# Kernel optimization log

Hardware: AMD Instinct MI355X
Metric: run time of the kernel (lower is better)

The kernel has to match this reference:

```python
import jax, jax.numpy as jnp
import numpy as np

B, S, D, M = 4, 8192, 1024, 512  # batch, seq_len, dim, memory_dim (= dim // 2)
LN_EPS = 1e-5


def _layernorm(z, g, b):
    mu = jnp.mean(z, axis=-1, keepdims=True)
    var = jnp.var(z, axis=-1, keepdims=True)
    return (z - mu) * jax.lax.rsqrt(var + LN_EPS) * g + b


def setup_inputs() -> dict:
    key = jax.random.key(0)
    ks = jax.random.split(key, 16)
    s_d = 1.0 / np.sqrt(D)
    s_m = 1.0 / np.sqrt(M)
    return {
        "x": jax.random.normal(ks[0], (B, S, D), jnp.float32),
        "Wd": jax.random.normal(ks[1], (D, M), jnp.float32) * s_d,
        "bd": jnp.zeros((M,), jnp.float32),
        "Wq": jax.random.normal(ks[2], (M, M), jnp.float32) * s_m,
        "bq": jnp.zeros((M,), jnp.float32),
        "Wk": jax.random.normal(ks[3], (M, M), jnp.float32) * s_m,
        "bk": jnp.zeros((M,), jnp.float32),
        "Wv": jax.random.normal(ks[4], (M, M), jnp.float32) * s_m,
        "bv": jnp.zeros((M,), jnp.float32),
        "gq": jnp.ones((M,), jnp.float32),
        "bq_ln": jnp.zeros((M,), jnp.float32),
        "gk": jnp.ones((M,), jnp.float32),
        "bk_ln": jnp.zeros((M,), jnp.float32),
        "W1": jax.random.normal(ks[5], (M, M), jnp.float32) * s_m,  # MemoryMLP layer 1
        "W2": jax.random.normal(ks[6], (M, M), jnp.float32) * s_m,  # MemoryMLP layer 2
        "Wu": jax.random.normal(ks[7], (M, D), jnp.float32) * s_m,
        "bu": jnp.zeros((D,), jnp.float32),
        "adaptive_lr": jnp.float32(0.01),
        "forget_factor": jnp.float32(0.1),
    }


def reference(x, Wd, bd, Wq, bq, Wk, bk, Wv, bv, gq, bq_ln, gk, bk_ln,
              W1, W2, Wu, bu, adaptive_lr, forget_factor):
    # project to memory dim: [B,S,M]
    h = jnp.einsum('bsd,dm->bsm', x, Wd) + bd
    q = _layernorm(h @ Wq + bq, gq, bq_ln)
    k = _layernorm(h @ Wk + bk, gk, bk_ln)
    v = h @ Wv + bv
    # MemoryMLP prediction on keys (depth 2, gelu between)
    pred = jax.nn.gelu(k @ W1) @ W2
    # surprise (negative gradient direction of MSE store loss), lr-scaled
    u = adaptive_lr * (v - pred)                       # inputs to scan [B,S,M]
    g = jax.nn.sigmoid(forget_factor)                  # scalar retention gate
    gates = jnp.full((B, S, 1), g, dtype=x.dtype)
    # gated linear recurrence s_t = g_t * s_{t-1} + u_t  (AssocScan math)
    def combine(a, c):
        g1, u1 = a
        g2, u2 = c
        return (g1 * g2, u1 * g2 + u2)
    _, mem = jax.lax.associative_scan(combine, (gates, u), axis=1)  # [B,S,M]
    # query-gated readout, project up, residual ('mal' integration)
    retrieved = q * mem
    out = x + jnp.einsum('bsm,md->bsd', retrieved, Wu) + bu
    return out
```

## Files before the change

kernel.cpp:

```cpp
#include <hip/hip_runtime.h>
#include <hip/hip_bf16.h>
#include <cstdint>


typedef unsigned short u16;
typedef unsigned int u32;
typedef __attribute__((ext_vector_type(8))) short short8;
typedef __attribute__((ext_vector_type(4))) float f32x4;

#define R_ROWS 32768
#define S_LEN 8192
#define D_DIM 1024
#define M_DIM 512

__device__ __forceinline__ float bf2f(u16 u) {
  union { unsigned int i; float f; } v; v.i = ((unsigned int)u) << 16; return v.f;
}
__device__ __forceinline__ u16 f2bf(float f) {
  union { float f; unsigned int i; } v; v.f = f;
  unsigned int r = v.i + 0x7fff + ((v.i >> 16) & 1);
  return (u16)(r >> 16);
}

__global__ __launch_bounds__(256)
void conv_f2b(const float* __restrict__ src, u16* __restrict__ dst) {
  const long i = ((long)blockIdx.x * 256 + threadIdx.x) * 8;
  short8 o;
#pragma unroll
  for (int j = 0; j < 8; ++j) o[j] = (short)f2bf(src[i + j]);
  *(short8*)(dst + i) = o;
}

__global__ __launch_bounds__(256)
void transpose_f2b(const float* __restrict__ src, u16* __restrict__ dst,
                   int rows, int cols) {
  __shared__ u16 tile[32][33];
  const int tx = threadIdx.x & 31;
  const int ty = threadIdx.x >> 5;
  const int bx = blockIdx.x, by = blockIdx.y;
  const int c = bx * 32 + tx;
#pragma unroll
  for (int i = 0; i < 32; i += 8)
    tile[ty + i][tx] = f2bf(src[(long)(by * 32 + ty + i) * cols + c]);
  __syncthreads();
  const int c2 = by * 32 + tx;
#pragma unroll
  for (int i = 0; i < 32; i += 8)
    dst[(long)(bx * 32 + ty + i) * rows + c2] = tile[tx][ty + i];
}

__global__ __launch_bounds__(256)
void concat3(const float* __restrict__ a, const float* __restrict__ b,
             const float* __restrict__ c, float* __restrict__ o) {
  const int i = blockIdx.x * 256 + threadIdx.x;
  o[i] = (i < 512) ? a[i] : (i < 1024) ? b[i - 512] : c[i - 1024];
}

template <int EPI>
__global__ __launch_bounds__(256, 2)
void gemm_bt(const u16* __restrict__ A, const u16* __restrict__ BT,
             const float* __restrict__ bias, void* __restrict__ Cv,
             const int K, const int N,
             const void* __restrict__ auxv, const float* __restrict__ sclr) {
  __shared__ __align__(16) short As[128 * 32];
  __shared__ __align__(16) short Bs[128 * 32];
  const int tid = threadIdx.x;
  const int lane = tid & 63;
  const int wid = tid >> 6;
  const int l15 = lane & 15;
  const int lg = lane >> 4;
  const int wr = wid >> 1;
  const int wc = wid & 1;
  const long am0 = (long)blockIdx.x * 128;
  const long bn0 = (long)blockIdx.y * 128;
  const int srow = tid >> 2;
  const int scol = (tid & 3) * 8;

  f32x4 acc[4][4];
#pragma unroll
  for (int i = 0; i < 4; ++i)
#pragma unroll
    for (int j = 0; j < 4; ++j) acc[i][j] = (f32x4){0.f, 0.f, 0.f, 0.f};

  for (int k0 = 0; k0 < K; k0 += 32) {
#pragma unroll
    for (int p = 0; p < 2; ++p) {
      const u16* ga = A + (am0 + p * 64 + srow) * K + (k0 + scol);
      const u16* gb = BT + (bn0 + p * 64 + srow) * K + (k0 + scol);
      char* la = ((char*)As) + p * 4096 + wid * 1024;
      char* lb = ((char*)Bs) + p * 4096 + wid * 1024;
      __builtin_amdgcn_global_load_lds(
          (const __attribute__((address_space(1))) void*)ga,
          (__attribute__((address_space(3))) void*)la, 16, 0, 0);
      __builtin_amdgcn_global_load_lds(
          (const __attribute__((address_space(1))) void*)gb,
          (__attribute__((address_space(3))) void*)lb, 16, 0, 0);
    }
    __syncthreads();
    short8 af[4], bf[4];
#pragma unroll
    for (int mi = 0; mi < 4; ++mi)
      af[mi] = *(const short8*)(As + (wr * 64 + mi * 16 + l15) * 32 + lg * 8);
#pragma unroll
    for (int ni = 0; ni < 4; ++ni)
      bf[ni] = *(const short8*)(Bs + (wc * 64 + ni * 16 + l15) * 32 + lg * 8);
#pragma unroll
    for (int mi = 0; mi < 4; ++mi)
#pragma unroll
      for (int ni = 0; ni < 4; ++ni)
        acc[mi][ni] = __builtin_amdgcn_mfma_f32_16x16x32_bf16(
            af[mi], bf[ni], acc[mi][ni], 0, 0, 0);
    __syncthreads();
  }

  if constexpr (EPI == 3) {
    __shared__ float Cs[32 * 132];
    const u16* xb = (const u16*)auxv;
    float* Of = (float*)Cv;
    const int trow = tid >> 5;
    const int tcol = (tid & 31) * 4;
#pragma unroll
    for (int p = 0; p < 4; ++p) {
      __syncthreads();
      if (wr == (p >> 1)) {
        const int mbase = (p & 1) * 2;
#pragma unroll
        for (int mm = 0; mm < 2; ++mm)
#pragma unroll
          for (int ni = 0; ni < 4; ++ni)
#pragma unroll
            for (int r = 0; r < 4; ++r)
              Cs[(mm * 16 + lg * 4 + r) * 132 + wc * 64 + ni * 16 + l15] =
                  acc[mbase + mm][ni][r];
      }
      __syncthreads();
#pragma unroll
      for (int rb = 0; rb < 32; rb += 8) {
        const int lrow = rb + trow;
        const long row = am0 + p * 32 + lrow;
        const long col = bn0 + tcol;
        f32x4 cv = *(const f32x4*)&Cs[lrow * 132 + tcol];
        const u32* xp = (const u32*)(xb + row * N + col);
        const u32 x0 = xp[0], x1 = xp[1];
        const f32x4 bv = *(const f32x4*)&bias[col];
        cv[0] += bf2f((u16)(x0 & 0xffff)) + bv[0];
        cv[1] += bf2f((u16)(x0 >> 16)) + bv[1];
        cv[2] += bf2f((u16)(x1 & 0xffff)) + bv[2];
        cv[3] += bf2f((u16)(x1 >> 16)) + bv[3];
        *(f32x4*)&Of[row * N + col] = cv;
      }
    }
    return;
  }

  float lr = 0.f;
  if (EPI == 2) lr = *sclr;
#pragma unroll
  for (int mi = 0; mi < 4; ++mi) {
    const long row0 = am0 + wr * 64 + mi * 16 + lg * 4;
#pragma unroll
    for (int ni = 0; ni < 4; ++ni) {
      const long col = bn0 + wc * 64 + ni * 16 + l15;
      const float bb = bias ? bias[col] : 0.f;
#pragma unroll
      for (int r = 0; r < 4; ++r) {
        const long row = row0 + r;
        float c = acc[mi][ni][r] + bb;
        if (EPI == 1) {
          c = 0.5f * c * (1.f + tanhf(0.7978845608028654f * (c + 0.044715f * c * c * c)));
        } else if (EPI == 2) {
          c = lr * (bf2f(((const u16*)auxv)[row * N + col]) - c);
        }
        if (EPI == 4) {
          const long sel = col >> 9;
          ((u16*)Cv)[sel * ((long)R_ROWS * M_DIM) + row * M_DIM + (col & 511)] =
              f2bf(c);
        } else {
          ((u16*)Cv)[row * N + col] = f2bf(c);
        }
      }
    }
  }
}

__global__ __launch_bounds__(256)
void ln_qk(u16* __restrict__ q, u16* __restrict__ k,
           const float* __restrict__ gq, const float* __restrict__ bq,
           const float* __restrict__ gk, const float* __restrict__ bk) {
  const int wid = threadIdx.x >> 6, lane = threadIdx.x & 63;
  long job = (long)blockIdx.x * 4 + wid;
  u16* base;
  const float *g, *b;
  if (job < R_ROWS) { base = q; g = gq; b = bq; }
  else { base = k; g = gk; b = bk; job -= R_ROWS; }
  u16* p = base + job * M_DIM + lane * 8;
  short8 zv = *(short8*)p;
  float z[8], s = 0.f, s2 = 0.f;
#pragma unroll
  for (int i = 0; i < 8; ++i) {
    z[i] = bf2f((u16)zv[i]);
    s += z[i];
    s2 += z[i] * z[i];
  }
#pragma unroll
  for (int off = 32; off >= 1; off >>= 1) {
    s += __shfl_xor(s, off);
    s2 += __shfl_xor(s2, off);
  }
  const float mu = s * (1.f / 512.f);
  const float inv = rsqrtf(s2 * (1.f / 512.f) - mu * mu + 1e-5f);
#pragma unroll
  for (int i = 0; i < 8; ++i) {
    float y = (z[i] - mu) * inv * g[lane * 8 + i] + b[lane * 8 + i];
    zv[i] = (short)f2bf(y);
  }
  *(short8*)p = zv;
}

#define SCAN_CH 32
#define SCAN_L (S_LEN / SCAN_CH)
#define SCAN_W 128

__global__ __launch_bounds__(256)
void scan_mul(const u16* __restrict__ u, const u16* __restrict__ q,
              u16* __restrict__ retr, const float* __restrict__ ffp) {
  const int m2 = threadIdx.x;
  const int b = blockIdx.x / SCAN_CH;
  const int ch = blockIdx.x % SCAN_CH;
  const float g = 1.f / (1.f + __expf(-*ffp));
  const long base = ((long)b * S_LEN) * M_DIM + 2 * m2;
  const int t0 = ch * SCAN_L;
  const int tw = (t0 >= SCAN_W) ? (t0 - SCAN_W) : 0;
  float s0 = 0.f, s1 = 0.f;
#pragma unroll 8
  for (int t = tw; t < t0; ++t) {
    const u32 w = *(const u32*)(u + base + (long)t * M_DIM);
    s0 = g * s0 + bf2f((u16)(w & 0xffff));
    s1 = g * s1 + bf2f((u16)(w >> 16));
  }
#pragma unroll 8
  for (int t = t0; t < t0 + SCAN_L; ++t) {
    const long idx = base + (long)t * M_DIM;
    const u32 w = *(const u32*)(u + idx);
    s0 = g * s0 + bf2f((u16)(w & 0xffff));
    s1 = g * s1 + bf2f((u16)(w >> 16));
    const u32 qw = *(const u32*)(q + idx);
    const u32 o = (u32)f2bf(bf2f((u16)(qw & 0xffff)) * s0) |
                  ((u32)f2bf(bf2f((u16)(qw >> 16)) * s1) << 16);
    *(u32*)(retr + idx) = o;
  }
}

extern "C" void kernel_launch(void* const* d_in, const int* in_sizes, int n_in,
                              void* d_out, int out_size, void* d_ws,
                              size_t ws_size, hipStream_t stream) {
  const float* x = (const float*)d_in[0];
  const float* Wd = (const float*)d_in[1];
  const float* bd = (const float*)d_in[2];
  const float* Wq = (const float*)d_in[3];
  const float* bq = (const float*)d_in[4];
  const float* Wk = (const float*)d_in[5];
  const float* bk = (const float*)d_in[6];
  const float* Wv = (const float*)d_in[7];
  const float* bv = (const float*)d_in[8];
  const float* gq = (const float*)d_in[9];
  const float* bq_ln = (const float*)d_in[10];
  const float* gk = (const float*)d_in[11];
  const float* bk_ln = (const float*)d_in[12];
  const float* W1 = (const float*)d_in[13];
  const float* W2 = (const float*)d_in[14];
  const float* Wu = (const float*)d_in[15];
  const float* bu = (const float*)d_in[16];
  const float* lr = (const float*)d_in[17];
  const float* ff = (const float*)d_in[18];

  char* w = (char*)d_ws;
  auto alloc = [&](size_t bytes) {
    char* p = w;
    w += (bytes + 255) & ~(size_t)255;
    return (u16*)p;
  };
  u16* WdT = alloc(512 * 1024 * 2);
  u16* WqkvT = alloc((size_t)1536 * 512 * 2);
  u16* W1T = alloc(512 * 512 * 2);
  u16* W2T = alloc(512 * 512 * 2);
  u16* WuT = alloc(1024 * 512 * 2);
  float* bqkv = (float*)alloc(1536 * 4);
  const size_t act = (size_t)R_ROWS * M_DIM * 2;
  u16* xb = alloc(2 * act);
  u16* hB = alloc(act);
  u16* qB = alloc(act);
  u16* kB = alloc(act);
  u16* vB = alloc(act);
  u16* t1 = hB;
  u16* uB = kB;
  u16* retr = vB;

  dim3 tb(256);
  conv_f2b<<<dim3(16384), tb, 0, stream>>>(x, xb);
  transpose_f2b<<<dim3(16, 32), tb, 0, stream>>>(Wd, WdT, 1024, 512);
  transpose_f2b<<<dim3(16, 16), tb, 0, stream>>>(Wq, WqkvT, 512, 512);
  transpose_f2b<<<dim3(16, 16), tb, 0, stream>>>(Wk, WqkvT + 512 * 512, 512, 512);
  transpose_f2b<<<dim3(16, 16), tb, 0, stream>>>(Wv, WqkvT + 2 * 512 * 512, 512, 512);
  transpose_f2b<<<dim3(16, 16), tb, 0, stream>>>(W1, W1T, 512, 512);
  transpose_f2b<<<dim3(16, 16), tb, 0, stream>>>(W2, W2T, 512, 512);
  transpose_f2b<<<dim3(32, 16), tb, 0, stream>>>(Wu, WuT, 512, 1024);
  concat3<<<dim3(6), tb, 0, stream>>>(bq, bk, bv, bqkv);

  gemm_bt<0><<<dim3(256, 4), 256, 0, stream>>>(xb, WdT, bd, hB, 1024, 512, nullptr, nullptr);
  gemm_bt<4><<<dim3(256, 12), 256, 0, stream>>>(hB, WqkvT, bqkv, qB, 512, 512, nullptr, nullptr);
  ln_qk<<<dim3(16384), 256, 0, stream>>>(qB, kB, gq, bq_ln, gk, bk_ln);
  gemm_bt<1><<<dim3(256, 4), 256, 0, stream>>>(kB, W1T, nullptr, t1, 512, 512, nullptr, nullptr);
  gemm_bt<2><<<dim3(256, 4), 256, 0, stream>>>(t1, W2T, nullptr, uB, 512, 512, vB, lr);
  scan_mul<<<dim3(4 * SCAN_CH), 256, 0, stream>>>(uB, qB, retr, ff);
  gemm_bt<3><<<dim3(256, 8), 256, 0, stream>>>(retr, WuT, bu, d_out, 512, 1024, xb, nullptr);
}
```

Before: 360.0 us.

## Add 256x256-tile double-buffered GEMM with direct global-to-LDS loads for bf16 GEMMs

Adds a new 512-thread GEMM kernel with 256x256 output tiles and a K-step of 64. It double-buffers LDS, fills it with global_load_lds so data skips registers, uses an XOR swizzle against bank conflicts, and interleaves fragment loads with MFMA groups under barriers and setprio. Four of the five bf16 GEMMs move to this kernel, while the output GEMM stays on the old 128x128 kernel, which now keeps only the EPI==3 epilogue. The aim is more data reuse per tile and overlap of loads with math. The costs are 128KB of LDS per block and fewer blocks: grids of 256, 768, 256 and 256 blocks, which may leave CUs underused or at low occupancy.

```diff
diff --git a/kernel.cpp b/kernel.cpp
--- a/kernel.cpp
+++ b/kernel.cpp
@@ -54,6 +54,180 @@
              const float* __restrict__ c, float* __restrict__ o) {
   const int i = blockIdx.x * 256 + threadIdx.x;
   o[i] = (i < 512) ? a[i] : (i < 1024) ? b[i - 512] : c[i - 1024];
+}
+
+template <int EPI>
+__global__ __launch_bounds__(512, 2)
+void gemm256(const u16* __restrict__ A, const u16* __restrict__ BT,
+             const float* __restrict__ bias, void* __restrict__ Cv,
+             const int K, const int N,
+             const void* __restrict__ auxv, const float* __restrict__ sclr) {
+  __shared__ __align__(16) char smem[131072];
+  const int tid = threadIdx.x;
+  const int lane = tid & 63;
+  const int wid = tid >> 6;
+  const int l15 = lane & 15;
+  const int lg = lane >> 4;
+  const int wm = wid >> 2;
+  const int wn = wid & 3;
+  const long am0 = (long)blockIdx.x * 256;
+  const long bn0 = (long)blockIdx.y * 256;
+  const int xl = ((l15 >> 2) & 1) << 4;
+  const int s_r = lane >> 3;
+  const int s_c = ((lane & 7) * 8) ^ (((lane >> 5) & 1) << 4);
+
+  char* const LA0 = smem;
+  char* const LB0 = smem + 32768;
+  char* const LA1 = smem + 65536;
+  char* const LB1 = smem + 98304;
+
+  f32x4 acc[8][4];
+#pragma unroll
+  for (int i = 0; i < 8; ++i)
+#pragma unroll
+    for (int j = 0; j < 4; ++j) acc[i][j] = (f32x4){0.f, 0.f, 0.f, 0.f};
+
+  const int NT = K >> 6;
+
+  auto stage = [&](char* ldsA, char* ldsB, int kt) {
+    const int k0 = kt << 6;
+#pragma unroll
+    for (int i = 0; i < 4; ++i) {
+      const int r = (wid * 4 + i) * 8 + s_r;
+      const u16* ga = A + (am0 + r) * (long)K + (k0 + s_c);
+      __builtin_amdgcn_global_load_lds(
+          (const __attribute__((address_space(1))) void*)ga,
+          (__attribute__((address_space(3))) void*)(ldsA + (wid * 4 + i) * 1024),
+          16, 0, 0);
+    }
+#pragma unroll
+    for (int i = 0; i < 4; ++i) {
+      const int r = (wid * 4 + i) * 8 + s_r;
+      const u16* gb = BT + (bn0 + r) * (long)K + (k0 + s_c);
+      __builtin_amdgcn_global_load_lds(
+          (const __attribute__((address_space(1))) void*)gb,
+          (__attribute__((address_space(3))) void*)(ldsB + (wid * 4 + i) * 1024),
+          16, 0, 0);
+    }
+  };
+
+  auto ldfrag = [&](const char* base, int Rbase, int kk) -> short8 {
+    return *(const short8*)(base + (long)(Rbase + l15) * 128 +
+                            (((kk << 5) + lg * 8) ^ xl) * 2);
+  };
+
+  auto tile_step = [&](char* cA, char* cB, char* nA, char* nB, int kstage) {
+    stage(nA, nB, kstage);
+    short8 a[4][2], b0[2][2], b1[2][2];
+#pragma unroll
+    for (int mi = 0; mi < 4; ++mi)
+#pragma unroll
+      for (int kk = 0; kk < 2; ++kk)
+        a[mi][kk] = ldfrag(cA, wm * 128 + mi * 16, kk);
+#pragma unroll
+    for (int ni = 0; ni < 2; ++ni)
+#pragma unroll
+      for (int kk = 0; kk < 2; ++kk)
+        b0[ni][kk] = ldfrag(cB, wn * 64 + ni * 16, kk);
+    __builtin_amdgcn_s_barrier();
+    __builtin_amdgcn_sched_barrier(0);
+    __builtin_amdgcn_s_setprio(1);
+#pragma unroll
+    for (int mi = 0; mi < 4; ++mi)
+#pragma unroll
+      for (int ni = 0; ni < 2; ++ni)
+#pragma unroll
+        for (int kk = 0; kk < 2; ++kk)
+          acc[mi][ni] = __builtin_amdgcn_mfma_f32_16x16x32_bf16(
+              a[mi][kk], b0[ni][kk], acc[mi][ni], 0, 0, 0);
+    __builtin_amdgcn_s_setprio(0);
+#pragma unroll
+    for (int ni = 0; ni < 2; ++ni)
+#pragma unroll
+      for (int kk = 0; kk < 2; ++kk)
+        b1[ni][kk] = ldfrag(cB, wn * 64 + (2 + ni) * 16, kk);
+    __builtin_amdgcn_s_barrier();
+    __builtin_amdgcn_sched_barrier(0);
+    __builtin_amdgcn_s_setprio(1);
+#pragma unroll
+    for (int mi = 0; mi < 4; ++mi)
+#pragma unroll
+      for (int ni = 0; ni < 2; ++ni)
+#pragma unroll
+        for (int kk = 0; kk < 2; ++kk)
+          acc[mi][2 + ni] = __builtin_amdgcn_mfma_f32_16x16x32_bf16(
+              a[mi][kk], b1[ni][kk], acc[mi][2 + ni], 0, 0, 0);
+    __builtin_amdgcn_s_setprio(0);
+#pragma unroll
+    for (int mi = 0; mi < 4; ++mi)
+#pragma unroll
+      for (int kk = 0; kk < 2; ++kk)
+        a[mi][kk] = ldfrag(cA, wm * 128 + (4 + mi) * 16, kk);
+    __builtin_amdgcn_s_barrier();
+    __builtin_amdgcn_sched_barrier(0);
+    __builtin_amdgcn_s_setprio(1);
+#pragma unroll
+    for (int mi = 0; mi < 4; ++mi)
+#pragma unroll
+      for (int ni = 0; ni < 2; ++ni)
+#pragma unroll
+        for (int kk = 0; kk < 2; ++kk)
+          acc[4 + mi][ni] = __builtin_amdgcn_mfma_f32_16x16x32_bf16(
+              a[mi][kk], b0[ni][kk], acc[4 + mi][ni], 0, 0, 0);
+    __builtin_amdgcn_s_setprio(0);
+    __builtin_amdgcn_s_barrier();
+    __builtin_amdgcn_sched_barrier(0);
+    __builtin_amdgcn_s_setprio(1);
+#pragma unroll
+    for (int mi = 0; mi < 4; ++mi)
+#pragma unroll
+      for (int ni = 0; ni < 2; ++ni)
+#pragma unroll
+        for (int kk = 0; kk < 2; ++kk)
+          acc[4 + mi][2 + ni] = __builtin_amdgcn_mfma_f32_16x16x32_bf16(
+              a[mi][kk], b1[ni][kk], acc[4 + mi][2 + ni], 0, 0, 0);
+    __builtin_amdgcn_s_setprio(0);
+    __syncthreads();
+  };
+
+  stage(LA0, LB0, 0);
+  __syncthreads();
+#pragma unroll 1
+  for (int t = 0; t < NT; t += 2) {
+    const int s1 = (t + 1 < NT) ? (t + 1) : (NT - 1);
+    const int s2 = (t + 2 < NT) ? (t + 2) : (NT - 1);
+    tile_step(LA0, LB0, LA1, LB1, s1);
+    tile_step(LA1, LB1, LA0, LB0, s2);
+  }
+
+  float lr = 0.f;
+  if (EPI == 2) lr = *sclr;
+#pragma unroll
+  for (int mi = 0; mi < 8; ++mi) {
+    const long row0 = am0 + wm * 128 + mi * 16 + lg * 4;
+#pragma unroll
+    for (int ni = 0; ni < 4; ++ni) {
+      const long col = bn0 + wn * 64 + ni * 16 + l15;
+      const float bb = bias ? bias[col] : 0.f;
+#pragma unroll
+      for (int r = 0; r < 4; ++r) {
+        const long row = row0 + r;
+        float c = acc[mi][ni][r] + bb;
+        if (EPI == 1) {
+          c = 0.5f * c * (1.f + tanhf(0.7978845608028654f * (c + 0.044715f * c * c * c)));
+        } else if (EPI == 2) {
+          c = lr * (bf2f(((const u16*)auxv)[row * N + col]) - c);
+        }
+        if (EPI == 4) {
+          const long sel = col >> 9;
+          ((u16*)Cv)[sel * ((long)R_ROWS * M_DIM) + row * M_DIM + (col & 511)] =
+              f2bf(c);
+        } else {
+          ((u16*)Cv)[row * N + col] = f2bf(c);
+        }
+      }
+    }
+  }
 }
 
 template <int EPI>
@@ -113,72 +287,40 @@
     __syncthreads();
   }
 
-  if constexpr (EPI == 3) {
-    __shared__ float Cs[32 * 132];
-    const u16* xb = (const u16*)auxv;
-    float* Of = (float*)Cv;
-    const int trow = tid >> 5;
-    const int tcol = (tid & 31) * 4;
-#pragma unroll
-    for (int p = 0; p < 4; ++p) {
-      __syncthreads();
-      if (wr == (p >> 1)) {
-        const int mbase = (p & 1) * 2;
-#pragma unroll
-        for (int mm = 0; mm < 2; ++mm)
-#pragma unroll
-          for (int ni = 0; ni < 4; ++ni)
-#pragma unroll
-            for (int r = 0; r < 4; ++r)
-              Cs[(mm * 16 + lg * 4 + r) * 132 + wc * 64 + ni * 16 + l15] =
-                  acc[mbase + mm][ni][r];
-      }
-      __syncthreads();
-#pragma unroll
-      for (int rb = 0; rb < 32; rb += 8) {
-        const int lrow = rb + trow;
-        const long row = am0 + p * 32 + lrow;
-        const long col = bn0 + tcol;
-        f32x4 cv = *(const f32x4*)&Cs[lrow * 132 + tcol];
-        const u32* xp = (const u32*)(xb + row * N + col);
-        const u32 x0 = xp[0], x1 = xp[1];
-        const f32x4 bv = *(const f32x4*)&bias[col];
-        cv[0] += bf2f((u16)(x0 & 0xffff)) + bv[0];
-        cv[1] += bf2f((u16)(x0 >> 16)) + bv[1];
-        cv[2] += bf2f((u16)(x1 & 0xffff)) + bv[2];
-        cv[3] += bf2f((u16)(x1 >> 16)) + bv[3];
-        *(f32x4*)&Of[row * N + col] = cv;
-      }
-    }
-    return;
-  }
-
-  float lr = 0.f;
-  if (EPI == 2) lr = *sclr;
-#pragma unroll
-  for (int mi = 0; mi < 4; ++mi) {
-    const long row0 = am0 + wr * 64 + mi * 16 + lg * 4;
-#pragma unroll
-    for (int ni = 0; ni < 4; ++ni) {
-      const long col = bn0 + wc * 64 + ni * 16 + l15;
-      const float bb = bias ? bias[col] : 0.f;
-#pragma unroll
-      for (int r = 0; r < 4; ++r) {
-        const long row = row0 + r;
-        float c = acc[mi][ni][r] + bb;
-        if (EPI == 1) {
-          c = 0.5f * c * (1.f + tanhf(0.7978845608028654f * (c + 0.044715f * c * c * c)));
-        } else if (EPI == 2) {
-          c = lr * (bf2f(((const u16*)auxv)[row * N + col]) - c);
-        }
-        if (EPI == 4) {
-          const long sel = col >> 9;
-          ((u16*)Cv)[sel * ((long)R_ROWS * M_DIM) + row * M_DIM + (col & 511)] =
-              f2bf(c);
-        } else {
-          ((u16*)Cv)[row * N + col] = f2bf(c);
-        }
-      }
+  __shared__ float Cs[32 * 132];
+  const u16* xb = (const u16*)auxv;
+  float* Of = (float*)Cv;
+  const int trow = tid >> 5;
+  const int tcol = (tid & 31) * 4;
+#pragma unroll
+  for (int p = 0; p < 4; ++p) {
+    __syncthreads();
+    if (wr == (p >> 1)) {
+      const int mbase = (p & 1) * 2;
+#pragma unroll
+      for (int mm = 0; mm < 2; ++mm)
+#pragma unroll
+        for (int ni = 0; ni < 4; ++ni)
+#pragma unroll
+          for (int r = 0; r < 4; ++r)
+            Cs[(mm * 16 + lg * 4 + r) * 132 + wc * 64 + ni * 16 + l15] =
+                acc[mbase + mm][ni][r];
+    }
+    __syncthreads();
+#pragma unroll
+    for (int rb = 0; rb < 32; rb += 8) {
+      const int lrow = rb + trow;
+      const long row = am0 + p * 32 + lrow;
+      const long col = bn0 + tcol;
+      f32x4 cv = *(const f32x4*)&Cs[lrow * 132 + tcol];
+      const u32* xp = (const u32*)(xb + row * N + col);
+      const u32 x0 = xp[0], x1 = xp[1];
+      const f32x4 bv = *(const f32x4*)&bias[col];
+      cv[0] += bf2f((u16)(x0 & 0xffff)) + bv[0];
+      cv[1] += bf2f((u16)(x0 >> 16)) + bv[1];
+      cv[2] += bf2f((u16)(x1 & 0xffff)) + bv[2];
+      cv[3] += bf2f((u16)(x1 >> 16)) + bv[3];
+      *(f32x4*)&Of[row * N + col] = cv;
     }
   }
 }
@@ -307,11 +449,11 @@
   transpose_f2b<<<dim3(32, 16), tb, 0, stream>>>(Wu, WuT, 512, 1024);
   concat3<<<dim3(6), tb, 0, stream>>>(bq, bk, bv, bqkv);
 
-  gemm_bt<0><<<dim3(256, 4), 256, 0, stream>>>(xb, WdT, bd, hB, 1024, 512, nullptr, nullptr);
-  gemm_bt<4><<<dim3(256, 12), 256, 0, stream>>>(hB, WqkvT, bqkv, qB, 512, 512, nullptr, nullptr);
+  gemm256<0><<<dim3(128, 2), 512, 0, stream>>>(xb, WdT, bd, hB, 1024, 512, nullptr, nullptr);
+  gemm256<4><<<dim3(128, 6), 512, 0, stream>>>(hB, WqkvT, bqkv, qB, 512, 512, nullptr, nullptr);
   ln_qk<<<dim3(16384), 256, 0, stream>>>(qB, kB, gq, bq_ln, gk, bk_ln);
-  gemm_bt<1><<<dim3(256, 4), 256, 0, stream>>>(kB, W1T, nullptr, t1, 512, 512, nullptr, nullptr);
-  gemm_bt<2><<<dim3(256, 4), 256, 0, stream>>>(t1, W2T, nullptr, uB, 512, 512, vB, lr);
+  gemm256<1><<<dim3(128, 2), 512, 0, stream>>>(kB, W1T, nullptr, t1, 512, 512, nullptr, nullptr);
+  gemm256<2><<<dim3(128, 2), 512, 0, stream>>>(t1, W2T, nullptr, uB, 512, 512, vB, lr);
   scan_mul<<<dim3(4 * SCAN_CH), 256, 0, stream>>>(uB, qB, retr, ff);
   gemm_bt<3><<<dim3(256, 8), 256, 0, stream>>>(retr, WuT, bu, d_out, 512, 1024, xb, nullptr);
 }
```

New measurement: 366.1 us. About the same (+1.7%).

## Add triple-buffered direct-to-LDS GEMM kernel for the inner bf16 GEMMs

Applied to the files above, without the earlier changes.

Adds a new GEMM kernel that uses 256x128 tiles with 512 threads, a K-step of 64 and three LDS buffers. Tiles are loaded with global_load_lds straight into XOR-swizzled shared memory, two stages ahead. The kernel waits on vmcnt instead of using full syncs and raises wave priority around the MFMA block. It replaces the old kernel for the down-projection, QKV, MLP1 and MLP2 GEMMs, while the old kernel is kept only for the final output GEMM with residual. The aim is to hide global load latency and avoid LDS bank conflicts. In exchange it uses about 144KB of LDS, so only one block fits per CU, which lowers occupancy.

```diff
diff --git a/kernel.cpp b/kernel.cpp
--- a/kernel.cpp
+++ b/kernel.cpp
@@ -54,6 +54,126 @@
              const float* __restrict__ c, float* __restrict__ o) {
   const int i = blockIdx.x * 256 + threadIdx.x;
   o[i] = (i < 512) ? a[i] : (i < 1024) ? b[i - 512] : c[i - 1024];
+}
+
+template <int EPI>
+__global__ __launch_bounds__(512, 1)
+void gemm_pipe(const u16* __restrict__ A, const u16* __restrict__ BT,
+               const float* __restrict__ bias, void* __restrict__ Cv,
+               const int K, const int N,
+               const void* __restrict__ auxv, const float* __restrict__ sclr) {
+  constexpr int BUFSZ = 49152;
+  __shared__ __align__(16) char smem[3 * BUFSZ];
+  const int tid = threadIdx.x;
+  const int lane = tid & 63;
+  const int wid = tid >> 6;
+  const int l15 = lane & 15;
+  const int lg = lane >> 4;
+  const int wm = wid >> 1;
+  const int wn = wid & 1;
+  const long am0 = (long)blockIdx.x * 256;
+  const long bn0 = (long)blockIdx.y * 128;
+  const int s_r = lane >> 3;
+  const int s_c = ((lane & 7) << 3) ^ ((lane >> 3) << 3);
+  const int xre = (l15 & 7) << 4;
+
+  f32x4 acc[4][4];
+#pragma unroll
+  for (int i = 0; i < 4; ++i)
+#pragma unroll
+    for (int j = 0; j < 4; ++j) acc[i][j] = (f32x4){0.f, 0.f, 0.f, 0.f};
+
+  const int NT = K >> 6;
+
+  auto stage = [&](int kt, int bi) {
+    char* bufA = smem + bi * BUFSZ;
+    char* bufB = bufA + 32768;
+    const int k0 = kt << 6;
+#pragma unroll
+    for (int i = 0; i < 4; ++i) {
+      const int j = wid * 4 + i;
+      const u16* ga = A + (am0 + j * 8 + s_r) * (long)K + (k0 + s_c);
+      __builtin_amdgcn_global_load_lds(
+          (const __attribute__((address_space(1))) void*)ga,
+          (__attribute__((address_space(3))) void*)(bufA + j * 1024), 16, 0, 0);
+    }
+#pragma unroll
+    for (int i = 0; i < 2; ++i) {
+      const int j = wid * 2 + i;
+      const u16* gb = BT + (bn0 + j * 8 + s_r) * (long)K + (k0 + s_c);
+      __builtin_amdgcn_global_load_lds(
+          (const __attribute__((address_space(1))) void*)gb,
+          (__attribute__((address_space(3))) void*)(bufB + j * 1024), 16, 0, 0);
+    }
+  };
+
+  stage(0, 0);
+  stage(1, 1);
+
+#pragma unroll 1
+  for (int t = 0; t < NT; ++t) {
+    __builtin_amdgcn_s_barrier();
+    const int ks = (t + 2 < NT) ? (t + 2) : (NT - 1);
+    stage(ks, (t + 2) % 3);
+    asm volatile("s_waitcnt vmcnt(12)" ::: "memory");
+    __builtin_amdgcn_s_barrier();
+    __builtin_amdgcn_sched_barrier(0);
+
+    const char* bufA = smem + (t % 3) * BUFSZ;
+    const char* bufB = bufA + 32768;
+    short8 a[4][2], b[4][2];
+#pragma unroll
+    for (int mi = 0; mi < 4; ++mi)
+#pragma unroll
+      for (int kk = 0; kk < 2; ++kk)
+        a[mi][kk] = *(const short8*)(bufA + (wm * 64 + mi * 16 + l15) * 128 +
+                                     ((kk * 64 + lg * 16) ^ xre));
+#pragma unroll
+    for (int ni = 0; ni < 4; ++ni)
+#pragma unroll
+      for (int kk = 0; kk < 2; ++kk)
+        b[ni][kk] = *(const short8*)(bufB + (wn * 64 + ni * 16 + l15) * 128 +
+                                     ((kk * 64 + lg * 16) ^ xre));
+    __builtin_amdgcn_s_setprio(1);
+#pragma unroll
+    for (int mi = 0; mi < 4; ++mi)
+#pragma unroll
+      for (int ni = 0; ni < 4; ++ni)
+#pragma unroll
+        for (int kk = 0; kk < 2; ++kk)
+          acc[mi][ni] = __builtin_amdgcn_mfma_f32_16x16x32_bf16(
+              a[mi][kk], b[ni][kk], acc[mi][ni], 0, 0, 0);
+    __builtin_amdgcn_s_setprio(0);
+  }
+
+  float lr = 0.f;
+  if (EPI == 2) lr = *sclr;
+#pragma unroll
+  for (int mi = 0; mi < 4; ++mi) {
+    const long row0 = am0 + wm * 64 + mi * 16 + lg * 4;
+#pragma unroll
+    for (int ni = 0; ni < 4; ++ni) {
+      const long col = bn0 + wn * 64 + ni * 16 + l15;
+      const float bb = bias ? bias[col] : 0.f;
+#pragma unroll
+      for (int r = 0; r < 4; ++r) {
+        const long row = row0 + r;
+        float c = acc[mi][ni][r] + bb;
+        if (EPI == 1) {
+          c = 0.5f * c * (1.f + tanhf(0.7978845608028654f * (c + 0.044715f * c * c * c)));
+        } else if (EPI == 2) {
+          c = lr * (bf2f(((const u16*)auxv)[row * N + col]) - c);
+        }
+        if (EPI == 4) {
+          const long sel = col >> 9;
+          ((u16*)Cv)[sel * ((long)R_ROWS * M_DIM) + row * M_DIM + (col & 511)] =
+              f2bf(c);
+        } else {
+          ((u16*)Cv)[row * N + col] = f2bf(c);
+        }
+      }
+    }
+  }
 }
 
 template <int EPI>
@@ -113,72 +233,40 @@
     __syncthreads();
   }
 
-  if constexpr (EPI == 3) {
-    __shared__ float Cs[32 * 132];
-    const u16* xb = (const u16*)auxv;
-    float* Of = (float*)Cv;
-    const int trow = tid >> 5;
-    const int tcol = (tid & 31) * 4;
-#pragma unroll
-    for (int p = 0; p < 4; ++p) {
-      __syncthreads();
-      if (wr == (p >> 1)) {
-        const int mbase = (p & 1) * 2;
-#pragma unroll
-        for (int mm = 0; mm < 2; ++mm)
-#pragma unroll
-          for (int ni = 0; ni < 4; ++ni)
-#pragma unroll
-            for (int r = 0; r < 4; ++r)
-              Cs[(mm * 16 + lg * 4 + r) * 132 + wc * 64 + ni * 16 + l15] =
-                  acc[mbase + mm][ni][r];
-      }
-      __syncthreads();
-#pragma unroll
-      for (int rb = 0; rb < 32; rb += 8) {
-        const int lrow = rb + trow;
-        const long row = am0 + p * 32 + lrow;
-        const long col = bn0 + tcol;
-        f32x4 cv = *(const f32x4*)&Cs[lrow * 132 + tcol];
-        const u32* xp = (const u32*)(xb + row * N + col);
-        const u32 x0 = xp[0], x1 = xp[1];
-        const f32x4 bv = *(const f32x4*)&bias[col];
-        cv[0] += bf2f((u16)(x0 & 0xffff)) + bv[0];
-        cv[1] += bf2f((u16)(x0 >> 16)) + bv[1];
-        cv[2] += bf2f((u16)(x1 & 0xffff)) + bv[2];
-        cv[3] += bf2f((u16)(x1 >> 16)) + bv[3];
-        *(f32x4*)&Of[row * N + col] = cv;
-      }
-    }
-    return;
-  }
-
-  float lr = 0.f;
-  if (EPI == 2) lr = *sclr;
-#pragma unroll
-  for (int mi = 0; mi < 4; ++mi) {
-    const long row0 = am0 + wr * 64 + mi * 16 + lg * 4;
-#pragma unroll
-    for (int ni = 0; ni < 4; ++ni) {
-      const long col = bn0 + wc * 64 + ni * 16 + l15;
-      const float bb = bias ? bias[col] : 0.f;
-#pragma unroll
-      for (int r = 0; r < 4; ++r) {
-        const long row = row0 + r;
-        float c = acc[mi][ni][r] + bb;
-        if (EPI == 1) {
-          c = 0.5f * c * (1.f + tanhf(0.7978845608028654f * (c + 0.044715f * c * c * c)));
-        } else if (EPI == 2) {
-          c = lr * (bf2f(((const u16*)auxv)[row * N + col]) - c);
-        }
-        if (EPI == 4) {
-          const long sel = col >> 9;
-          ((u16*)Cv)[sel * ((long)R_ROWS * M_DIM) + row * M_DIM + (col & 511)] =
-              f2bf(c);
-        } else {
-          ((u16*)Cv)[row * N + col] = f2bf(c);
-        }
-      }
+  __shared__ float Cs[32 * 132];
+  const u16* xb = (const u16*)auxv;
+  float* Of = (float*)Cv;
+  const int trow = tid >> 5;
+  const int tcol = (tid & 31) * 4;
+#pragma unroll
+  for (int p = 0; p < 4; ++p) {
+    __syncthreads();
+    if (wr == (p >> 1)) {
+      const int mbase = (p & 1) * 2;
+#pragma unroll
+      for (int mm = 0; mm < 2; ++mm)
+#pragma unroll
+        for (int ni = 0; ni < 4; ++ni)
+#pragma unroll
+          for (int r = 0; r < 4; ++r)
+            Cs[(mm * 16 + lg * 4 + r) * 132 + wc * 64 + ni * 16 + l15] =
+                acc[mbase + mm][ni][r];
+    }
+    __syncthreads();
+#pragma unroll
+    for (int rb = 0; rb < 32; rb += 8) {
+      const int lrow = rb + trow;
+      const long row = am0 + p * 32 + lrow;
+      const long col = bn0 + tcol;
+      f32x4 cv = *(const f32x4*)&Cs[lrow * 132 + tcol];
+      const u32* xp = (const u32*)(xb + row * N + col);
+      const u32 x0 = xp[0], x1 = xp[1];
+      const f32x4 bv = *(const f32x4*)&bias[col];
+      cv[0] += bf2f((u16)(x0 & 0xffff)) + bv[0];
+      cv[1] += bf2f((u16)(x0 >> 16)) + bv[1];
+      cv[2] += bf2f((u16)(x1 & 0xffff)) + bv[2];
+      cv[3] += bf2f((u16)(x1 >> 16)) + bv[3];
+      *(f32x4*)&Of[row * N + col] = cv;
     }
   }
 }
@@ -307,11 +395,11 @@
   transpose_f2b<<<dim3(32, 16), tb, 0, stream>>>(Wu, WuT, 512, 1024);
   concat3<<<dim3(6), tb, 0, stream>>>(bq, bk, bv, bqkv);
 
-  gemm_bt<0><<<dim3(256, 4), 256, 0, stream>>>(xb, WdT, bd, hB, 1024, 512, nullptr, nullptr);
-  gemm_bt<4><<<dim3(256, 12), 256, 0, stream>>>(hB, WqkvT, bqkv, qB, 512, 512, nullptr, nullptr);
+  gemm_pipe<0><<<dim3(128, 4), 512, 0, stream>>>(xb, WdT, bd, hB, 1024, 512, nullptr, nullptr);
+  gemm_pipe<4><<<dim3(128, 12), 512, 0, stream>>>(hB, WqkvT, bqkv, qB, 512, 512, nullptr, nullptr);
   ln_qk<<<dim3(16384), 256, 0, stream>>>(qB, kB, gq, bq_ln, gk, bk_ln);
-  gemm_bt<1><<<dim3(256, 4), 256, 0, stream>>>(kB, W1T, nullptr, t1, 512, 512, nullptr, nullptr);
-  gemm_bt<2><<<dim3(256, 4), 256, 0, stream>>>(t1, W2T, nullptr, uB, 512, 512, vB, lr);
+  gemm_pipe<1><<<dim3(128, 4), 512, 0, stream>>>(kB, W1T, nullptr, t1, 512, 512, nullptr, nullptr);
+  gemm_pipe<2><<<dim3(128, 4), 512, 0, stream>>>(t1, W2T, nullptr, uB, 512, 512, vB, lr);
   scan_mul<<<dim3(4 * SCAN_CH), 256, 0, stream>>>(uB, qB, retr, ff);
   gemm_bt<3><<<dim3(256, 8), 256, 0, stream>>>(retr, WuT, bu, d_out, 512, 1024, xb, nullptr);
 }
```

New measurement: 390.7 us. +8.5%, slower.

## Swizzle GEMM LDS tiles and merge weight preparation kernels into one launch

Applied to the files above, without the earlier changes.

Applies an XOR swizzle to the 16-byte chunk position within each 32-element LDS row in the bf16 GEMM, both when loading via global_load_lds and when reading MFMA fragments, to reduce LDS bank conflicts. Also fuses the seven weight transpose kernels and the bias concat into a single launch to cut launch overhead. The swizzle adds a little index arithmetic and must stay consistent between writer and reader.

```diff
diff --git a/kernel.cpp b/kernel.cpp
--- a/kernel.cpp
+++ b/kernel.cpp
@@ -32,12 +32,48 @@
 }
 
 __global__ __launch_bounds__(256)
-void transpose_f2b(const float* __restrict__ src, u16* __restrict__ dst,
-                   int rows, int cols) {
+void prep_weights(const float* __restrict__ Wd, const float* __restrict__ Wq,
+                  const float* __restrict__ Wk, const float* __restrict__ Wv,
+                  const float* __restrict__ W1, const float* __restrict__ W2,
+                  const float* __restrict__ Wu, const float* __restrict__ bq,
+                  const float* __restrict__ bk, const float* __restrict__ bv,
+                  u16* __restrict__ WdT, u16* __restrict__ WqkvT,
+                  u16* __restrict__ W1T, u16* __restrict__ W2T,
+                  u16* __restrict__ WuT, float* __restrict__ bqkv) {
   __shared__ u16 tile[32][33];
+  int id = blockIdx.x;
+  if (id >= 2304) {
+    const int i = (id - 2304) * 256 + threadIdx.x;
+    bqkv[i] = (i < 512) ? bq[i] : (i < 1024) ? bk[i - 512] : bv[i - 1024];
+    return;
+  }
+  const float* src;
+  u16* dst;
+  int rows, cols, bx, by;
+  if (id < 512) {
+    src = Wd; dst = WdT; rows = 1024; cols = 512;
+    bx = id & 15; by = id >> 4;
+  } else if (id < 768) {
+    src = Wq; dst = WqkvT; rows = 512; cols = 512;
+    id -= 512; bx = id & 15; by = id >> 4;
+  } else if (id < 1024) {
+    src = Wk; dst = WqkvT + 512 * 512; rows = 512; cols = 512;
+    id -= 768; bx = id & 15; by = id >> 4;
+  } else if (id < 1280) {
+    src = Wv; dst = WqkvT + 2 * 512 * 512; rows = 512; cols = 512;
+    id -= 1024; bx = id & 15; by = id >> 4;
+  } else if (id < 1536) {
+    src = W1; dst = W1T; rows = 512; cols = 512;
+    id -= 1280; bx = id & 15; by = id >> 4;
+  } else if (id < 1792) {
+    src = W2; dst = W2T; rows = 512; cols = 512;
+    id -= 1536; bx = id & 15; by = id >> 4;
+  } else {
+    src = Wu; dst = WuT; rows = 512; cols = 1024;
+    id -= 1792; bx = id & 31; by = id >> 5;
+  }
   const int tx = threadIdx.x & 31;
   const int ty = threadIdx.x >> 5;
-  const int bx = blockIdx.x, by = blockIdx.y;
   const int c = bx * 32 + tx;
 #pragma unroll
   for (int i = 0; i < 32; i += 8)
@@ -47,13 +83,6 @@
 #pragma unroll
   for (int i = 0; i < 32; i += 8)
     dst[(long)(bx * 32 + ty + i) * rows + c2] = tile[tx][ty + i];
-}
-
-__global__ __launch_bounds__(256)
-void concat3(const float* __restrict__ a, const float* __restrict__ b,
-             const float* __restrict__ c, float* __restrict__ o) {
-  const int i = blockIdx.x * 256 + threadIdx.x;
-  o[i] = (i < 512) ? a[i] : (i < 1024) ? b[i - 512] : c[i - 1024];
 }
 
 template <int EPI>
@@ -74,7 +103,9 @@
   const long am0 = (long)blockIdx.x * 128;
   const long bn0 = (long)blockIdx.y * 128;
   const int srow = tid >> 2;
-  const int scol = (tid & 3) * 8;
+  const int sxor = (srow >> 1) & 3;
+  const int scol = ((tid & 3) ^ sxor) << 3;
+  const int rchunk = (lg ^ ((l15 >> 1) & 3)) << 3;
 
   f32x4 acc[4][4];
 #pragma unroll
@@ -100,10 +131,10 @@
     short8 af[4], bf[4];
 #pragma unroll
     for (int mi = 0; mi < 4; ++mi)
-      af[mi] = *(const short8*)(As + (wr * 64 + mi * 16 + l15) * 32 + lg * 8);
+      af[mi] = *(const short8*)(As + (wr * 64 + mi * 16 + l15) * 32 + rchunk);
 #pragma unroll
     for (int ni = 0; ni < 4; ++ni)
-      bf[ni] = *(const short8*)(Bs + (wc * 64 + ni * 16 + l15) * 32 + lg * 8);
+      bf[ni] = *(const short8*)(Bs + (wc * 64 + ni * 16 + l15) * 32 + rchunk);
 #pragma unroll
     for (int mi = 0; mi < 4; ++mi)
 #pragma unroll
@@ -298,14 +329,9 @@
 
   dim3 tb(256);
   conv_f2b<<<dim3(16384), tb, 0, stream>>>(x, xb);
-  transpose_f2b<<<dim3(16, 32), tb, 0, stream>>>(Wd, WdT, 1024, 512);
-  transpose_f2b<<<dim3(16, 16), tb, 0, stream>>>(Wq, WqkvT, 512, 512);
-  transpose_f2b<<<dim3(16, 16), tb, 0, stream>>>(Wk, WqkvT + 512 * 512, 512, 512);
-  transpose_f2b<<<dim3(16, 16), tb, 0, stream>>>(Wv, WqkvT + 2 * 512 * 512, 512, 512);
-  transpose_f2b<<<dim3(16, 16), tb, 0, stream>>>(W1, W1T, 512, 512);
-  transpose_f2b<<<dim3(16, 16), tb, 0, stream>>>(W2, W2T, 512, 512);
-  transpose_f2b<<<dim3(32, 16), tb, 0, stream>>>(Wu, WuT, 512, 1024);
-  concat3<<<dim3(6), tb, 0, stream>>>(bq, bk, bv, bqkv);
+  prep_weights<<<dim3(2310), tb, 0, stream>>>(Wd, Wq, Wk, Wv, W1, W2, Wu,
+                                              bq, bk, bv,
+                                              WdT, WqkvT, W1T, W2T, WuT, bqkv);
 
   gemm_bt<0><<<dim3(256, 4), 256, 0, stream>>>(xb, WdT, bd, hB, 1024, 512, nullptr, nullptr);
   gemm_bt<4><<<dim3(256, 12), 256, 0, stream>>>(hB, WqkvT, bqkv, qB, 512, 512, nullptr, nullptr);
```

After: 350.1 us. -2.8%, faster.
